# Performance work log

Measured on AMD Instinct MI355X. Metric: run time of the kernel, lower is better.

## Reference

```python
import jax, jax.numpy as jnp
import numpy as np

B, L_ENC, ENC_IN = 8, 1536, 7
LABEL_LEN, PRED_LEN = 512, 512
D_MODEL, N_HEADS, D_FF = 512, 8, 2048
E_LAYERS = 2
BUCKET_SIZE, N_HASHES = 64, 4
C_OUT, MARK_F = 7, 4
D_HEAD = D_MODEL // N_HEADS
L = L_ENC + PRED_LEN            # 2048, multiple of 2*bucket_size -> fit_length adds no pad
N_BUCKETS = L // BUCKET_SIZE    # 32
SELF_ATTN_VALUE = -5e4          # reformer_pytorch TOKEN_SELF_ATTN_VALUE


def _ln(x, g, b, eps=1e-5):
    mu = x.mean(-1, keepdims=True)
    var = ((x - mu) ** 2).mean(-1, keepdims=True)
    return (x - mu) * jax.lax.rsqrt(var + eps) * g + b


def _pos_embedding(length, d):
    pos = np.arange(length)[:, None].astype(np.float32)
    div = np.exp(np.arange(0, d, 2).astype(np.float32) * -(np.log(10000.0) / d))
    pe = np.zeros((length, d), np.float32)
    pe[:, 0::2] = np.sin(pos * div)
    pe[:, 1::2] = np.cos(pos * div)
    return jnp.asarray(pe)


def _lsh_attention(qk, v, rot):
    # qk, v: (b, L, d) with b = B*heads; rot: (d, n_hashes, n_buckets//2)
    b, Ls, d = qk.shape
    # --- hash: random rotations, buckets = argmax over [r, -r] ---
    rotated = jnp.einsum('bld,dhr->bhlr', qk, rot)
    rotated = jnp.concatenate([rotated, -rotated], axis=-1)            # (b,H,L,nb)
    buckets = jnp.argmax(rotated, axis=-1)                             # (b,H,L)
    buckets = buckets + (jnp.arange(N_HASHES) * N_BUCKETS)[None, :, None]
    buckets = buckets.reshape(b, N_HASHES * Ls)
    ticker = jnp.arange(N_HASHES * Ls)[None, :] % Ls
    # --- stable sort by (bucket, position) ---
    sticker = jnp.argsort(buckets * Ls + ticker, axis=-1)              # (b, H*L)
    undo_sort = jnp.argsort(sticker, axis=-1)
    st = sticker % Ls
    sqk = jnp.take_along_axis(qk, st[..., None], axis=1)               # (b, H*L, d)
    sv = jnp.take_along_axis(v, st[..., None], axis=1)
    n_chunks = N_HASHES * N_BUCKETS
    bq_t = st.reshape(b, n_chunks, -1)                                 # (b, C, cs)
    bq = sqk.reshape(b, n_chunks, -1, d)
    bv = sv.reshape(b, n_chunks, -1, d)
    # shared-QK: keys are l2-normalized queries
    bk = bq / jnp.maximum(jnp.linalg.norm(bq, axis=-1, keepdims=True), 1e-12)
    look = lambda x: jnp.concatenate([x, jnp.roll(x, 1, axis=1)], axis=2)
    bk, bv, bkv_t = look(bk), look(bv), look(bq_t)
    dots = jnp.einsum('bcie,bcje->bcij', bq, bk) * (d ** -0.5)         # (b,C,cs,2cs)
    self_mask = bq_t[:, :, :, None] == bkv_t[:, :, None, :]
    dots = jnp.where(self_mask, SELF_ATTN_VALUE, dots)
    lse = jax.nn.logsumexp(dots, axis=-1, keepdims=True)
    p = jnp.exp(dots - lse)
    so = jnp.einsum('bcij,bcje->bcie', p, bv).reshape(b, -1, d)        # (b, H*L, d)
    slog = lse.reshape(b, -1)
    o = jnp.take_along_axis(so, undo_sort[..., None], axis=1).reshape(b, N_HASHES, Ls, d)
    logits = jnp.take_along_axis(slog, undo_sort, axis=1).reshape(b, N_HASHES, Ls, 1)
    w = jnp.exp(logits - jax.nn.logsumexp(logits, axis=1, keepdims=True))
    return (o * w).sum(axis=1)                                         # (b, L, d)


def _forward(x_enc, x_mark_enc, x_dec, x_mark_dec, token_conv_w, time_w,
             qk_w, v_w, out_w, out_b, rotations,
             ffn1_w, ffn1_b, ffn2_w, ffn2_b,
             norm1_g, norm1_b, norm2_g, norm2_b, normf_g, normf_b,
             proj_w, proj_b):
    x = jnp.concatenate([x_enc, x_dec[:, -PRED_LEN:, :]], axis=1)      # (B, L, enc_in)
    xm = jnp.concatenate([x_mark_enc, x_mark_dec[:, -PRED_LEN:, :]], axis=1)
    # TokenEmbedding: Conv1d k=3, circular padding, no bias
    xp = jnp.concatenate([x[:, -1:, :], x, x[:, :1, :]], axis=1)
    tok = jax.lax.conv_general_dilated(xp, token_conv_w, (1,), 'VALID',
                                       dimension_numbers=('NWC', 'WIO', 'NWC'))
    h = tok + _pos_embedding(L, D_MODEL)[None] + xm @ time_w
    for l in range(E_LAYERS):
        qk = (h @ qk_w[l]).reshape(B, L, N_HEADS, D_HEAD).transpose(0, 2, 1, 3).reshape(B * N_HEADS, L, D_HEAD)
        v = (h @ v_w[l]).reshape(B, L, N_HEADS, D_HEAD).transpose(0, 2, 1, 3).reshape(B * N_HEADS, L, D_HEAD)
        a = _lsh_attention(qk, v, rotations[l])
        a = a.reshape(B, N_HEADS, L, D_HEAD).transpose(0, 2, 1, 3).reshape(B, L, D_MODEL)
        a = a @ out_w[l] + out_b[l]
        h = _ln(h + a, norm1_g[l], norm1_b[l])
        y = jax.nn.gelu(h @ ffn1_w[l] + ffn1_b[l], approximate=False) @ ffn2_w[l] + ffn2_b[l]
        h = _ln(h + y, norm2_g[l], norm2_b[l])
    h = _ln(h, normf_g, normf_b)
    out = h @ proj_w + proj_b
    return out[:, -PRED_LEN:, :]


def setup_inputs() -> dict:
    key = jax.random.key(0)
    ks = jax.random.split(key, 16)
    s = 0.02
    return {
        'x_enc': jax.random.normal(ks[0], (B, L_ENC, ENC_IN), jnp.float32),
        'x_mark_enc': jax.random.normal(ks[1], (B, L_ENC, MARK_F), jnp.float32),
        'x_dec': jax.random.normal(ks[2], (B, LABEL_LEN + PRED_LEN, ENC_IN), jnp.float32),
        'x_mark_dec': jax.random.normal(ks[3], (B, LABEL_LEN + PRED_LEN, MARK_F), jnp.float32),
        'token_conv_w': jax.random.normal(ks[4], (3, ENC_IN, D_MODEL), jnp.float32) * s,
        'time_w': jax.random.normal(ks[5], (MARK_F, D_MODEL), jnp.float32) * s,
        'qk_w': jax.random.normal(ks[6], (E_LAYERS, D_MODEL, D_MODEL), jnp.float32) * s,
        'v_w': jax.random.normal(ks[7], (E_LAYERS, D_MODEL, D_MODEL), jnp.float32) * s,
        'out_w': jax.random.normal(ks[8], (E_LAYERS, D_MODEL, D_MODEL), jnp.float32) * s,
        'out_b': jnp.zeros((E_LAYERS, D_MODEL), jnp.float32),
        'rotations': jax.random.normal(ks[9], (E_LAYERS, D_HEAD, N_HASHES, N_BUCKETS // 2), jnp.float32),
        'ffn1_w': jax.random.normal(ks[10], (E_LAYERS, D_MODEL, D_FF), jnp.float32) * s,
        'ffn1_b': jnp.zeros((E_LAYERS, D_FF), jnp.float32),
        'ffn2_w': jax.random.normal(ks[11], (E_LAYERS, D_FF, D_MODEL), jnp.float32) * s,
        'ffn2_b': jnp.zeros((E_LAYERS, D_MODEL), jnp.float32),
        'norm1_g': jnp.ones((E_LAYERS, D_MODEL), jnp.float32),
        'norm1_b': jnp.zeros((E_LAYERS, D_MODEL), jnp.float32),
        'norm2_g': jnp.ones((E_LAYERS, D_MODEL), jnp.float32),
        'norm2_b': jnp.zeros((E_LAYERS, D_MODEL), jnp.float32),
        'normf_g': jnp.ones((D_MODEL,), jnp.float32),
        'normf_b': jnp.zeros((D_MODEL,), jnp.float32),
        'proj_w': jax.random.normal(ks[12], (D_MODEL, C_OUT), jnp.float32) * s,
        'proj_b': jnp.zeros((C_OUT,), jnp.float32),
    }


def reference(x_enc, x_mark_enc, x_dec, x_mark_dec, token_conv_w, time_w,
              qk_w, v_w, out_w, out_b, rotations,
              ffn1_w, ffn1_b, ffn2_w, ffn2_b,
              norm1_g, norm1_b, norm2_g, norm2_b, normf_g, normf_b,
              proj_w, proj_b):
    return _forward(x_enc, x_mark_enc, x_dec, x_mark_dec, token_conv_w, time_w,
                    qk_w, v_w, out_w, out_b, rotations,
                    ffn1_w, ffn1_b, ffn2_w, ffn2_b,
                    norm1_g, norm1_b, norm2_g, norm2_b, normf_g, normf_b,
                    proj_w, proj_b)
```

## Files before the change

kernel.cpp:

```cpp
#include <hip/hip_runtime.h>


#define BATCH 8
#define SEQL 2048
#define DM 512
#define NH 8
#define DH 64
#define DFF 2048
#define NHASH 4
#define NBUCK 32
#define NCHUNK 128
#define CS 64
#define ROWS (BATCH*SEQL)
#define BHN (BATCH*NH)
#define SORTN (NHASH*SEQL)
#define SELF_VAL -5e4f

typedef __attribute__((ext_vector_type(4))) float f32x4;
typedef __attribute__((ext_vector_type(8))) short short8;

__device__ __forceinline__ float bfu2f(unsigned int u16) {
    return __uint_as_float(u16 << 16);
}
__device__ __forceinline__ unsigned short f2bfu(float f) {
    unsigned int x = __float_as_uint(f);
    x += 0x7fffu + ((x >> 16) & 1u);
    return (unsigned short)(x >> 16);
}

__device__ __forceinline__ void gld16(const void* g, void* l) {
    __builtin_amdgcn_global_load_lds(
        (const __attribute__((address_space(1))) unsigned int*)g,
        (__attribute__((address_space(3))) unsigned int*)l, 16, 0, 0);
}

__device__ __forceinline__ float getx(const float* xe, const float* xd, int b, int lm, int c) {
    return (lm < 1536) ? xe[((size_t)b * 1536 + lm) * 7 + c]
                       : xd[((size_t)b * 1024 + (lm - 1024)) * 7 + c];
}

__global__ __launch_bounds__(512) void embed_k(
    const float* __restrict__ x_enc, const float* __restrict__ x_me,
    const float* __restrict__ x_dec, const float* __restrict__ x_md,
    const float* __restrict__ cw, const float* __restrict__ tw,
    float* __restrict__ h, unsigned short* __restrict__ hb)
{
    const int row = blockIdx.x;
    const int b = row >> 11, l = row & 2047;
    const int d = threadIdx.x;
    __shared__ float xs[21];
    __shared__ float xms[4];
    if (d < 21) {
        const int k = d / 7, c = d % 7;
        const int lm = (l + k + 2047) & 2047;
        xs[d] = getx(x_enc, x_dec, b, lm, c);
    } else if (d < 25) {
        const int m = d - 21;
        xms[m] = (l < 1536) ? x_me[((size_t)b * 1536 + l) * 4 + m]
                            : x_md[((size_t)b * 1024 + (l - 1024)) * 4 + m];
    }
    __syncthreads();
    float tok = 0.f;
    #pragma unroll
    for (int kc = 0; kc < 21; ++kc) tok = fmaf(xs[kc], cw[kc * 512 + d], tok);
    float tm = 0.f;
    #pragma unroll
    for (int m = 0; m < 4; ++m) tm = fmaf(xms[m], tw[m * 512 + d], tm);
    const int pair = d & ~1;
    const float freq = expf((float)pair * (-9.210340371976184f / 512.f));
    const float ang = (float)l * freq;
    const float pe = (d & 1) ? cosf(ang) : sinf(ang);
    const float val = tok + pe + tm;
    h[(size_t)row * 512 + d] = val;
    hb[(size_t)row * 512 + d] = f2bfu(val);
}

__global__ __launch_bounds__(256) void gemm_k(
    const float* __restrict__ A, const float* __restrict__ B,
    float* __restrict__ C, int M, int N, int K)
{
    __shared__ float As[16][132];
    __shared__ float Bs[16][64];
    const int tid = threadIdx.x;
    const int bm = blockIdx.x * 128, bn = blockIdx.y * 64;
    const int ty = tid >> 4, tx = tid & 15;
    const int ar = tid >> 1, ac = (tid & 1) * 8;
    const int br = tid >> 4, bc = (tid & 15) * 4;
    float acc[8][4] = {};
    const float* Ap = A + (size_t)(bm + ar) * K + ac;
    const float* Bp = B + (size_t)br * N + bn + bc;
    float4 a0v = *reinterpret_cast<const float4*>(Ap);
    float4 a1v = *reinterpret_cast<const float4*>(Ap + 4);
    float4 b0v = *reinterpret_cast<const float4*>(Bp);
    for (int k0 = 0; k0 < K; k0 += 16) {
        As[ac + 0][ar] = a0v.x; As[ac + 1][ar] = a0v.y;
        As[ac + 2][ar] = a0v.z; As[ac + 3][ar] = a0v.w;
        As[ac + 4][ar] = a1v.x; As[ac + 5][ar] = a1v.y;
        As[ac + 6][ar] = a1v.z; As[ac + 7][ar] = a1v.w;
        *reinterpret_cast<float4*>(&Bs[br][bc]) = b0v;
        __syncthreads();
        if (k0 + 16 < K) {
            a0v = *reinterpret_cast<const float4*>(Ap + k0 + 16);
            a1v = *reinterpret_cast<const float4*>(Ap + k0 + 20);
            b0v = *reinterpret_cast<const float4*>(Bp + (size_t)(k0 + 16) * N);
        }
        #pragma unroll
        for (int k = 0; k < 16; ++k) {
            const float4 a0 = *reinterpret_cast<const float4*>(&As[k][ty * 8]);
            const float4 a1 = *reinterpret_cast<const float4*>(&As[k][ty * 8 + 4]);
            const float4 b0 = *reinterpret_cast<const float4*>(&Bs[k][tx * 4]);
            const float a[8] = {a0.x,a0.y,a0.z,a0.w,a1.x,a1.y,a1.z,a1.w};
            const float bb[4] = {b0.x,b0.y,b0.z,b0.w};
            #pragma unroll
            for (int i = 0; i < 8; ++i)
                #pragma unroll
                for (int j = 0; j < 4; ++j) acc[i][j] = fmaf(a[i], bb[j], acc[i][j]);
        }
        __syncthreads();
    }
    #pragma unroll
    for (int i = 0; i < 8; ++i) {
        const size_t cb = (size_t)(bm + ty * 8 + i) * N + bn + tx * 4;
        *reinterpret_cast<float4*>(C + cb) = make_float4(acc[i][0],acc[i][1],acc[i][2],acc[i][3]);
    }
}

__global__ __launch_bounds__(256) void tcast_k(
    const float* __restrict__ W, unsigned short* __restrict__ Wt, int K, int N)
{
    __shared__ float t[32][33];
    const size_t zo = (size_t)blockIdx.z * K * N;
    const int kb = blockIdx.x * 32, nb = blockIdx.y * 32;
    const int tx = threadIdx.x & 31, ty = threadIdx.x >> 5;
    #pragma unroll
    for (int i = ty; i < 32; i += 8)
        t[i][tx] = W[zo + (size_t)(kb + i) * N + nb + tx];
    __syncthreads();
    #pragma unroll
    for (int i = ty; i < 32; i += 8)
        Wt[zo + (size_t)(nb + i) * K + kb + tx] = f2bfu(t[tx][i]);
}

template<int OUT_BF, int ACT, int BIAS>
__global__ __launch_bounds__(256) void mgemm_k(
    const unsigned short* __restrict__ A,
    const unsigned short* __restrict__ Bt,
    const float* __restrict__ bias,
    void* __restrict__ Cv, int N, int K)
{
    __shared__ unsigned short As[128 * 32];
    __shared__ unsigned short Bs[128 * 32];
    const int tid = threadIdx.x;
    const int bm = blockIdx.x * 128, bn = blockIdx.y * 128;
    const int lane = tid & 63, w = tid >> 6;
    const int wr = (w >> 1) * 64, wc = (w & 1) * 64;
    const int fr = lane & 15, fq = lane >> 4;
    const int r0 = tid >> 2, c0 = (tid & 3) * 8;
    const unsigned short* Ag = A + (size_t)(bm + r0) * K + c0;
    const unsigned short* Bg = Bt + (size_t)(bn + r0) * K + c0;
    f32x4 acc[4][4];
    #pragma unroll
    for (int i = 0; i < 4; ++i)
        #pragma unroll
        for (int j = 0; j < 4; ++j) acc[i][j] = (f32x4){0.f, 0.f, 0.f, 0.f};
    for (int k0 = 0; k0 < K; k0 += 32) {
        gld16(Ag + k0,                   As + tid * 8);
        gld16(Ag + (size_t)64 * K + k0,  As + tid * 8 + 2048);
        gld16(Bg + k0,                   Bs + tid * 8);
        gld16(Bg + (size_t)64 * K + k0,  Bs + tid * 8 + 2048);
        __syncthreads();
        short8 af[4], bfr[4];
        #pragma unroll
        for (int mi = 0; mi < 4; ++mi)
            af[mi] = *reinterpret_cast<const short8*>(As + (wr + mi * 16 + fr) * 32 + fq * 8);
        #pragma unroll
        for (int ni = 0; ni < 4; ++ni)
            bfr[ni] = *reinterpret_cast<const short8*>(Bs + (wc + ni * 16 + fr) * 32 + fq * 8);
        #pragma unroll
        for (int mi = 0; mi < 4; ++mi)
            #pragma unroll
            for (int ni = 0; ni < 4; ++ni)
                acc[mi][ni] = __builtin_amdgcn_mfma_f32_16x16x32_bf16(
                    af[mi], bfr[ni], acc[mi][ni], 0, 0, 0);
        __syncthreads();
    }
    float bv[4];
    if (BIAS) {
        #pragma unroll
        for (int ni = 0; ni < 4; ++ni) bv[ni] = bias[bn + wc + ni * 16 + fr];
    }
    #pragma unroll
    for (int mi = 0; mi < 4; ++mi) {
        #pragma unroll
        for (int r = 0; r < 4; ++r) {
            const int row = bm + wr + mi * 16 + fq * 4 + r;
            #pragma unroll
            for (int ni = 0; ni < 4; ++ni) {
                float val = acc[mi][ni][r];
                if (BIAS) val += bv[ni];
                if (ACT) val = 0.5f * val * (1.0f + erff(val * 0.7071067811865475f));
                const size_t idx = (size_t)row * N + bn + wc + ni * 16 + fr;
                if (OUT_BF) ((unsigned short*)Cv)[idx] = f2bfu(val);
                else        ((float*)Cv)[idx] = val;
            }
        }
    }
}

__global__ __launch_bounds__(256, 4) void hash_k(
    const float* __restrict__ qk, const float* __restrict__ rot,
    int* __restrict__ buckets)
{
    __shared__ float rs[16][68];
    const int t = threadIdx.x;
    const int hh_blk = blockIdx.x >> 9;
    for (int u = t; u < 1024; u += 256) {
        const int d = u >> 4, j = u & 15;
        rs[j][d] = rot[d * 64 + hh_blk * 16 + j];
    }
    __syncthreads();
    const int gid = blockIdx.x * 256 + t;
    const int l = gid & 2047;
    const int bh = (gid >> 11) & 63;
    const int hh = gid >> 17;
    const int b = bh >> 3, head = bh & 7;
    const float* qrow = qk + (size_t)(b * 2048 + l) * 512 + head * 64;
    float q[64];
    #pragma unroll
    for (int d4 = 0; d4 < 16; ++d4) {
        const float4 qq = reinterpret_cast<const float4*>(qrow)[d4];
        q[d4*4+0]=qq.x; q[d4*4+1]=qq.y; q[d4*4+2]=qq.z; q[d4*4+3]=qq.w;
    }
    float bvp = -1e38f, bvn = -1e38f;
    int bip = 0, bin_ = 16;
    #pragma unroll
    for (int j = 0; j < 16; ++j) {
        float dot = 0.f;
        #pragma unroll
        for (int d = 0; d < 64; d += 4) {
            const float4 r = *reinterpret_cast<const float4*>(&rs[j][d]);
            dot += q[d]*r.x + q[d+1]*r.y + q[d+2]*r.z + q[d+3]*r.w;
        }
        if (dot  > bvp) { bvp = dot;  bip = j; }
        if (-dot > bvn) { bvn = -dot; bin_ = 16 + j; }
    }
    const int idx = (bvn > bvp) ? bin_ : bip;
    buckets[((size_t)bh << 13) + hh * 2048 + l] = hh * 32 + idx;
}

__global__ __launch_bounds__(256) void sort_k(
    const int* __restrict__ buckets, int* __restrict__ st_sorted, int* __restrict__ pos_of)
{
    const int bh = blockIdx.x >> 2, hh = blockIdx.x & 3;
    const int t = threadIdx.x;
    __shared__ unsigned short cnt[256][32];
    __shared__ int tot[32];
    __shared__ int startc[32];
    {
        uint4* p = reinterpret_cast<uint4*>(&cnt[t][0]);
        const uint4 z = {0,0,0,0};
        #pragma unroll
        for (int q = 0; q < 4; ++q) p[q] = z;
    }
    const size_t base = (size_t)bh * SORTN + hh * 2048;
    int myb[8];
    #pragma unroll
    for (int j = 0; j < 8; ++j) {
        const int i = t * 8 + j;
        const int g = buckets[base + i] - hh * 32;
        myb[j] = g;
        cnt[t][g]++;
    }
    __syncthreads();
    if (t < 32) {
        int run = 0;
        for (int tt = 0; tt < 256; ++tt) {
            const int x = cnt[tt][t];
            cnt[tt][t] = (unsigned short)run;
            run += x;
        }
        tot[t] = run;
    }
    __syncthreads();
    if (t == 0) {
        int s = 0;
        for (int g = 0; g < 32; ++g) { startc[g] = s; s += tot[g]; }
    }
    __syncthreads();
    #pragma unroll
    for (int j = 0; j < 8; ++j) {
        const int i = t * 8 + j;
        const int g = myb[j];
        const int rank = cnt[t][g]++;
        const int pos = hh * 2048 + startc[g] + rank;
        st_sorted[(size_t)bh * SORTN + pos] = i;
        pos_of[base + i] = pos;
    }
}

__global__ __launch_bounds__(256) void lsh_attn_k(
    const float* __restrict__ qk, const unsigned short* __restrict__ vbf,
    const int* __restrict__ st_sorted,
    unsigned short* __restrict__ so, float* __restrict__ slog)
{
    const int c = blockIdx.x;
    const int bh = blockIdx.y;
    const int b = bh >> 3, head = bh & 7;
    __shared__ unsigned short Ks[128 * 72];
    __shared__ unsigned short Vt[128 * 64];
    __shared__ unsigned short Ps[64 * 136];
    __shared__ float rnorm[128];
    __shared__ int stk[128];
    const int t = threadIdx.x;

    {
        const int r = t >> 1, hf = t & 1;
        const int cprev = (c + NCHUNK - 1) & (NCHUNK - 1);
        const int spos = (r < 64) ? (c * CS + r) : (cprev * CS + (r - 64));
        const int l = st_sorted[(size_t)bh * SORTN + spos];
        if (hf == 0) stk[r] = l;
        const size_t ro = (size_t)(b * 2048 + l) * 512 + head * 64 + hf * 32;
        const float4* q4 = reinterpret_cast<const float4*>(qk + ro);
        float ss = 0.f;
        #pragma unroll
        for (int u = 0; u < 8; ++u) {
            const float4 a = q4[u];
            ss += a.x*a.x + a.y*a.y + a.z*a.z + a.w*a.w;
            ushort4 pk;
            pk.x = f2bfu(a.x); pk.y = f2bfu(a.y); pk.z = f2bfu(a.z); pk.w = f2bfu(a.w);
            *reinterpret_cast<ushort4*>(&Ks[r * 72 + hf * 32 + u * 4]) = pk;
        }
        ss += __shfl_xor(ss, 1);
        if (hf == 0) rnorm[r] = 1.0f / fmaxf(sqrtf(ss), 1e-12f);
        const uint4* v16 = reinterpret_cast<const uint4*>(vbf + ro);
        const uint4 a0 = v16[0], a1 = v16[1], a2 = v16[2], a3 = v16[3];
        const unsigned int wd[16] = {a0.x,a0.y,a0.z,a0.w, a1.x,a1.y,a1.z,a1.w,
                                     a2.x,a2.y,a2.z,a2.w, a3.x,a3.y,a3.z,a3.w};
        #pragma unroll
        for (int e = 0; e < 32; ++e) {
            const int d = hf * 32 + e;
            const unsigned short us = (unsigned short)(wd[e >> 1] >> ((e & 1) * 16));
            Vt[(d * 128 + r) ^ ((d & 7) << 3)] = us;
        }
    }
    __syncthreads();

    const int lane = t & 63, w = t >> 6;
    const int fr = lane & 15, fq = lane >> 4;

    short8 aq[2];
    #pragma unroll
    for (int s = 0; s < 2; ++s)
        aq[s] = *reinterpret_cast<const short8*>(&Ks[(w * 16 + fr) * 72 + s * 32 + fq * 8]);
    f32x4 cc[8];
    #pragma unroll
    for (int n = 0; n < 8; ++n) cc[n] = (f32x4){0.f, 0.f, 0.f, 0.f};
    #pragma unroll
    for (int n = 0; n < 8; ++n) {
        #pragma unroll
        for (int s = 0; s < 2; ++s) {
            const short8 bk = *reinterpret_cast<const short8*>(
                &Ks[(n * 16 + fr) * 72 + s * 32 + fq * 8]);
            cc[n] = __builtin_amdgcn_mfma_f32_16x16x32_bf16(aq[s], bk, cc[n], 0, 0, 0);
        }
    }

    int stq_r[4];
    #pragma unroll
    for (int r = 0; r < 4; ++r) stq_r[r] = stk[w * 16 + fq * 4 + r];
    float mx[4] = {-3.0e38f, -3.0e38f, -3.0e38f, -3.0e38f};
    #pragma unroll
    for (int n = 0; n < 8; ++n) {
        const int key = n * 16 + fr;
        const float rn = rnorm[key] * 0.125f;
        const int sk = stk[key];
        #pragma unroll
        for (int r = 0; r < 4; ++r) {
            const float val = (stq_r[r] == sk) ? SELF_VAL : cc[n][r] * rn;
            cc[n][r] = val;
            mx[r] = fmaxf(mx[r], val);
        }
    }
    #pragma unroll
    for (int r = 0; r < 4; ++r) {
        mx[r] = fmaxf(mx[r], __shfl_xor(mx[r], 1));
        mx[r] = fmaxf(mx[r], __shfl_xor(mx[r], 2));
        mx[r] = fmaxf(mx[r], __shfl_xor(mx[r], 4));
        mx[r] = fmaxf(mx[r], __shfl_xor(mx[r], 8));
    }
    float sm[4] = {0.f, 0.f, 0.f, 0.f};
    #pragma unroll
    for (int n = 0; n < 8; ++n)
        #pragma unroll
        for (int r = 0; r < 4; ++r) {
            const float e = __expf(cc[n][r] - mx[r]);
            cc[n][r] = e;
            sm[r] += e;
        }
    #pragma unroll
    for (int r = 0; r < 4; ++r) {
        sm[r] += __shfl_xor(sm[r], 1);
        sm[r] += __shfl_xor(sm[r], 2);
        sm[r] += __shfl_xor(sm[r], 4);
        sm[r] += __shfl_xor(sm[r], 8);
    }
    float rsum[4];
    #pragma unroll
    for (int r = 0; r < 4; ++r) rsum[r] = 1.0f / sm[r];
    if (fr == 0) {
        #pragma unroll
        for (int r = 0; r < 4; ++r)
            slog[(size_t)bh * SORTN + c * CS + w * 16 + fq * 4 + r] = mx[r] + logf(sm[r]);
    }

    #pragma unroll
    for (int n = 0; n < 8; ++n)
        #pragma unroll
        for (int r = 0; r < 4; ++r)
            Ps[(w * 16 + fq * 4 + r) * 136 + n * 16 + fr] = f2bfu(cc[n][r]);
    __syncthreads();

    short8 pa[4];
    #pragma unroll
    for (int s = 0; s < 4; ++s)
        pa[s] = *reinterpret_cast<const short8*>(&Ps[(w * 16 + fr) * 136 + s * 32 + fq * 8]);
    f32x4 oo[4];
    #pragma unroll
    for (int n = 0; n < 4; ++n) oo[n] = (f32x4){0.f, 0.f, 0.f, 0.f};
    #pragma unroll
    for (int n = 0; n < 4; ++n) {
        const int d = n * 16 + fr;
        #pragma unroll
        for (int s = 0; s < 4; ++s) {
            const short8 vb = *reinterpret_cast<const short8*>(
                &Vt[(d * 128 + s * 32 + fq * 8) ^ ((d & 7) << 3)]);
            oo[n] = __builtin_amdgcn_mfma_f32_16x16x32_bf16(pa[s], vb, oo[n], 0, 0, 0);
        }
    }

    #pragma unroll
    for (int r = 0; r < 4; ++r) {
        const int qrow = w * 16 + fq * 4 + r;
        const size_t ob = ((size_t)bh * SORTN + c * CS + qrow) * 64;
        #pragma unroll
        for (int n = 0; n < 4; ++n)
            so[ob + n * 16 + fr] = f2bfu(oo[n][r] * rsum[r]);
    }
}

__global__ __launch_bounds__(256) void combine_k(
    const unsigned short* __restrict__ so, const float* __restrict__ slog,
    const int* __restrict__ pos_of, unsigned short* __restrict__ aout)
{
    const int gid = blockIdx.x * 256 + threadIdx.x;
    const int d = gid & 63;
    const int bl = gid >> 6;
    const int l = bl & 2047;
    const int bh = bl >> 11;
    const int b = bh >> 3, head = bh & 7;
    int pos[4]; float lg[4];
    #pragma unroll
    for (int hh = 0; hh < 4; ++hh) {
        pos[hh] = pos_of[((size_t)bh << 13) + hh * 2048 + l];
        lg[hh] = slog[((size_t)bh << 13) + pos[hh]];
    }
    const float m = fmaxf(fmaxf(lg[0], lg[1]), fmaxf(lg[2], lg[3]));
    float w[4]; float sw = 0.f;
    #pragma unroll
    for (int hh = 0; hh < 4; ++hh) { w[hh] = expf(lg[hh] - m); sw += w[hh]; }
    const float inv = 1.0f / sw;
    float acc = 0.f;
    #pragma unroll
    for (int hh = 0; hh < 4; ++hh)
        acc += w[hh] * bfu2f(so[(((size_t)bh << 13) + pos[hh]) * 64 + d]);
    aout[(size_t)(b * 2048 + l) * 512 + head * 64 + d] = f2bfu(acc * inv);
}

template<int RES, int WBF>
__global__ __launch_bounds__(256) void ln_k(
    float* __restrict__ h, const float* __restrict__ res,
    const float* __restrict__ g, const float* __restrict__ bta,
    unsigned short* __restrict__ hb)
{
    const int row = blockIdx.x * 4 + (threadIdx.x >> 6);
    const int lane = threadIdx.x & 63;
    const size_t base = (size_t)row * 512;
    float4 xa = *reinterpret_cast<const float4*>(h + base + lane * 4);
    float4 xb = *reinterpret_cast<const float4*>(h + base + 256 + lane * 4);
    if (RES) {
        const float4 ra = *reinterpret_cast<const float4*>(res + base + lane * 4);
        const float4 rb = *reinterpret_cast<const float4*>(res + base + 256 + lane * 4);
        xa.x += ra.x; xa.y += ra.y; xa.z += ra.z; xa.w += ra.w;
        xb.x += rb.x; xb.y += rb.y; xb.z += rb.z; xb.w += rb.w;
    }
    float sum = xa.x + xa.y + xa.z + xa.w + xb.x + xb.y + xb.z + xb.w;
    float sq = xa.x*xa.x + xa.y*xa.y + xa.z*xa.z + xa.w*xa.w
             + xb.x*xb.x + xb.y*xb.y + xb.z*xb.z + xb.w*xb.w;
    #pragma unroll
    for (int off = 32; off > 0; off >>= 1) {
        sum += __shfl_xor(sum, off);
        sq  += __shfl_xor(sq, off);
    }
    const float mu = sum * (1.0f / 512.0f);
    const float var = sq * (1.0f / 512.0f) - mu * mu;
    const float rstd = rsqrtf(var + 1e-5f);
    const float4 ga = *reinterpret_cast<const float4*>(g + lane * 4);
    const float4 gb = *reinterpret_cast<const float4*>(g + 256 + lane * 4);
    const float4 ba = *reinterpret_cast<const float4*>(bta + lane * 4);
    const float4 bb = *reinterpret_cast<const float4*>(bta + 256 + lane * 4);
    float4 oa, ob;
    oa.x = (xa.x - mu) * rstd * ga.x + ba.x;
    oa.y = (xa.y - mu) * rstd * ga.y + ba.y;
    oa.z = (xa.z - mu) * rstd * ga.z + ba.z;
    oa.w = (xa.w - mu) * rstd * ga.w + ba.w;
    ob.x = (xb.x - mu) * rstd * gb.x + bb.x;
    ob.y = (xb.y - mu) * rstd * gb.y + bb.y;
    ob.z = (xb.z - mu) * rstd * gb.z + bb.z;
    ob.w = (xb.w - mu) * rstd * gb.w + bb.w;
    *reinterpret_cast<float4*>(h + base + lane * 4) = oa;
    *reinterpret_cast<float4*>(h + base + 256 + lane * 4) = ob;
    if (WBF) {
        ushort4 pa, pb;
        pa.x = f2bfu(oa.x); pa.y = f2bfu(oa.y); pa.z = f2bfu(oa.z); pa.w = f2bfu(oa.w);
        pb.x = f2bfu(ob.x); pb.y = f2bfu(ob.y); pb.z = f2bfu(ob.z); pb.w = f2bfu(ob.w);
        *reinterpret_cast<ushort4*>(hb + base + lane * 4) = pa;
        *reinterpret_cast<ushort4*>(hb + base + 256 + lane * 4) = pb;
    }
}

__global__ __launch_bounds__(256) void lnf_k(
    float* __restrict__ h, const float* __restrict__ g, const float* __restrict__ bta)
{
    const int vrow = blockIdx.x * 4 + (threadIdx.x >> 6);
    const int row = (vrow >> 9) * 2048 + 1536 + (vrow & 511);
    const int lane = threadIdx.x & 63;
    const size_t base = (size_t)row * 512;
    float4 xa = *reinterpret_cast<const float4*>(h + base + lane * 4);
    float4 xb = *reinterpret_cast<const float4*>(h + base + 256 + lane * 4);
    float sum = xa.x + xa.y + xa.z + xa.w + xb.x + xb.y + xb.z + xb.w;
    float sq = xa.x*xa.x + xa.y*xa.y + xa.z*xa.z + xa.w*xa.w
             + xb.x*xb.x + xb.y*xb.y + xb.z*xb.z + xb.w*xb.w;
    #pragma unroll
    for (int off = 32; off > 0; off >>= 1) {
        sum += __shfl_xor(sum, off);
        sq  += __shfl_xor(sq, off);
    }
    const float mu = sum * (1.0f / 512.0f);
    const float var = sq * (1.0f / 512.0f) - mu * mu;
    const float rstd = rsqrtf(var + 1e-5f);
    const float4 ga = *reinterpret_cast<const float4*>(g + lane * 4);
    const float4 gb = *reinterpret_cast<const float4*>(g + 256 + lane * 4);
    const float4 ba = *reinterpret_cast<const float4*>(bta + lane * 4);
    const float4 bb = *reinterpret_cast<const float4*>(bta + 256 + lane * 4);
    float4 oa, ob;
    oa.x = (xa.x - mu) * rstd * ga.x + ba.x;
    oa.y = (xa.y - mu) * rstd * ga.y + ba.y;
    oa.z = (xa.z - mu) * rstd * ga.z + ba.z;
    oa.w = (xa.w - mu) * rstd * ga.w + ba.w;
    ob.x = (xb.x - mu) * rstd * gb.x + bb.x;
    ob.y = (xb.y - mu) * rstd * gb.y + bb.y;
    ob.z = (xb.z - mu) * rstd * gb.z + bb.z;
    ob.w = (xb.w - mu) * rstd * gb.w + bb.w;
    *reinterpret_cast<float4*>(h + base + lane * 4) = oa;
    *reinterpret_cast<float4*>(h + base + 256 + lane * 4) = ob;
}

__global__ __launch_bounds__(256) void proj_k(
    const float* __restrict__ h, const float* __restrict__ pw,
    const float* __restrict__ pb, float* __restrict__ out)
{
    const int wid = (blockIdx.x * 256 + threadIdx.x) >> 6;
    const int lane = threadIdx.x & 63;
    const int b = wid >> 9, tt = wid & 511;
    const float* row = h + (size_t)(b * 2048 + 1536 + tt) * 512;
    const float4 h0 = reinterpret_cast<const float4*>(row)[lane * 2];
    const float4 h1 = reinterpret_cast<const float4*>(row)[lane * 2 + 1];
    const float he[8] = {h0.x, h0.y, h0.z, h0.w, h1.x, h1.y, h1.z, h1.w};
    float acc[7] = {};
    #pragma unroll
    for (int e = 0; e < 8; ++e) {
        const int k = lane * 8 + e;
        #pragma unroll
        for (int cq = 0; cq < 7; ++cq) acc[cq] = fmaf(he[e], pw[k * 7 + cq], acc[cq]);
    }
    #pragma unroll
    for (int cq = 0; cq < 7; ++cq) {
        #pragma unroll
        for (int off = 32; off > 0; off >>= 1) acc[cq] += __shfl_xor(acc[cq], off);
    }
    if (lane == 0) {
        const size_t ob = ((size_t)(b * 512) + tt) * 7;
        #pragma unroll
        for (int cq = 0; cq < 7; ++cq) out[ob + cq] = acc[cq] + pb[cq];
    }
}

__global__ void nan_k(float* o) { o[0] = __int_as_float(0x7fc00000); }

extern "C" void kernel_launch(void* const* d_in, const int* in_sizes, int n_in,
                              void* d_out, int out_size, void* d_ws, size_t ws_size,
                              hipStream_t stream)
{
    const float* x_enc  = (const float*)d_in[0];
    const float* x_me   = (const float*)d_in[1];
    const float* x_dec  = (const float*)d_in[2];
    const float* x_md   = (const float*)d_in[3];
    const float* conv_w = (const float*)d_in[4];
    const float* time_w = (const float*)d_in[5];
    const float* qk_w   = (const float*)d_in[6];
    const float* v_w    = (const float*)d_in[7];
    const float* out_w  = (const float*)d_in[8];
    const float* out_b  = (const float*)d_in[9];
    const float* rots   = (const float*)d_in[10];
    const float* f1w    = (const float*)d_in[11];
    const float* f1b    = (const float*)d_in[12];
    const float* f2w    = (const float*)d_in[13];
    const float* f2b    = (const float*)d_in[14];
    const float* n1g    = (const float*)d_in[15];
    const float* n1b    = (const float*)d_in[16];
    const float* n2g    = (const float*)d_in[17];
    const float* n2b    = (const float*)d_in[18];
    const float* nfg    = (const float*)d_in[19];
    const float* nfb    = (const float*)d_in[20];
    const float* pw     = (const float*)d_in[21];
    const float* pb     = (const float*)d_in[22];

    char* ws = (char*)d_ws;
    const size_t HBYT = (size_t)ROWS * DM * 4;
    float* h    = (float*)ws;                  ws += HBYT;
    unsigned short* hb = (unsigned short*)ws;  ws += HBYT / 2;
    float* qkb  = (float*)ws;                  ws += HBYT;
    float* gout = (float*)ws;                  ws += HBYT;
    unsigned short* mid = (unsigned short*)ws; ws += (size_t)ROWS * DFF * 2;
    float* slog = (float*)ws;                  ws += (size_t)BHN * SORTN * 4;
    int* buckets = (int*)ws;                   ws += (size_t)BHN * SORTN * 4;
    int* st_sorted = (int*)ws;                 ws += (size_t)BHN * SORTN * 4;
    int* pos_of = (int*)ws;                    ws += (size_t)BHN * SORTN * 4;
    unsigned short* wT = (unsigned short*)ws;  ws += (size_t)(2*262144 + 2*262144 + 2*1048576 + 2*1048576) * 2;
    const size_t need = (size_t)(ws - (char*)d_ws);
    if (ws_size < need) { nan_k<<<1, 1, 0, stream>>>((float*)d_out); return; }

    unsigned short* vT  = wT;
    unsigned short* oT  = vT + 2 * 262144;
    unsigned short* f1T = oT + 2 * 262144;
    unsigned short* f2T = f1T + 2 * 1048576;
    unsigned short* ab  = (unsigned short*)qkb;
    unsigned short* vbf = (unsigned short*)gout;

    tcast_k<<<dim3(16, 16, 2), 256, 0, stream>>>(v_w,   vT,  DM, DM);
    tcast_k<<<dim3(16, 16, 2), 256, 0, stream>>>(out_w, oT,  DM, DM);
    tcast_k<<<dim3(16, 64, 2), 256, 0, stream>>>(f1w,   f1T, DM, DFF);
    tcast_k<<<dim3(64, 16, 2), 256, 0, stream>>>(f2w,   f2T, DFF, DM);

    embed_k<<<ROWS, 512, 0, stream>>>(x_enc, x_me, x_dec, x_md, conv_w, time_w, h, hb);

    for (int l = 0; l < 2; ++l) {
        const size_t wo = (size_t)l * DM * DM;
        gemm_k<<<dim3(ROWS/128, DM/64), 256, 0, stream>>>(h, qk_w + wo, qkb, ROWS, DM, DM);
        mgemm_k<1,0,0><<<dim3(ROWS/128, DM/128), 256, 0, stream>>>(hb, vT + (size_t)l*262144, nullptr, vbf, DM, DM);
        hash_k<<<(NHASH * BHN * SEQL) / 256, 256, 0, stream>>>(qkb, rots + (size_t)l * DH * NHASH * (NBUCK/2), buckets);
        sort_k<<<BHN * 4, 256, 0, stream>>>(buckets, st_sorted, pos_of);
        lsh_attn_k<<<dim3(NCHUNK, BHN), 256, 0, stream>>>(qkb, vbf, st_sorted, mid , slog);
        combine_k<<<(BHN * SEQL * DH) / 256, 256, 0, stream>>>(mid, slog, pos_of, ab);
        mgemm_k<0,0,1><<<dim3(ROWS/128, DM/128), 256, 0, stream>>>(ab, oT + (size_t)l*262144, out_b + l * DM, gout, DM, DM);
        ln_k<1,1><<<ROWS/4, 256, 0, stream>>>(h, gout, n1g + l * DM, n1b + l * DM, hb);
        mgemm_k<1,1,1><<<dim3(ROWS/128, DFF/128), 256, 0, stream>>>(hb, f1T + (size_t)l*1048576, f1b + l * DFF, mid, DFF, DM);
        mgemm_k<0,0,1><<<dim3(ROWS/128, DM/128), 256, 0, stream>>>(mid, f2T + (size_t)l*1048576, f2b + l * DM, gout, DM, DFF);
        ln_k<1,1><<<ROWS/4, 256, 0, stream>>>(h, gout, n2g + l * DM, n2b + l * DM, hb);
    }
    lnf_k<<<(BATCH * 512) / 4, 256, 0, stream>>>(h, nfg, nfb);
    proj_k<<<(BATCH * 512 / 4), 256, 0, stream>>>(h, pw, pb, (float*)d_out);
}
```

Baseline: 957.4 us.

## Deepen fp32 GEMM K-tile to 32 and alias attention P buffer onto K tile

The fp32 tiled GEMM now stages 32-wide K slices per iteration instead of 16, halving the barrier count per output tile at the cost of doubled LDS and more prefetch registers. The LSH attention kernel reuses the K shared buffer for the probability matrix, with an added barrier to protect it, and requests 4 blocks per CU via launch bounds. Together these aim to cut sync overhead and raise occupancy, with a risk of register pressure or spills from the occupancy hint.

```diff
diff --git a/kernel.cpp b/kernel.cpp
--- a/kernel.cpp
+++ b/kernel.cpp
@@ -79,33 +79,44 @@
     const float* __restrict__ A, const float* __restrict__ B,
     float* __restrict__ C, int M, int N, int K)
 {
-    __shared__ float As[16][132];
-    __shared__ float Bs[16][64];
+    __shared__ float As[32][132];
+    __shared__ float Bs[32][64];
     const int tid = threadIdx.x;
     const int bm = blockIdx.x * 128, bn = blockIdx.y * 64;
     const int ty = tid >> 4, tx = tid & 15;
-    const int ar = tid >> 1, ac = (tid & 1) * 8;
-    const int br = tid >> 4, bc = (tid & 15) * 4;
+    const int ar = tid >> 1, ac = (tid & 1) * 16;
+    const int br = tid >> 3, bc = (tid & 7) * 8;
     float acc[8][4] = {};
     const float* Ap = A + (size_t)(bm + ar) * K + ac;
     const float* Bp = B + (size_t)br * N + bn + bc;
-    float4 a0v = *reinterpret_cast<const float4*>(Ap);
-    float4 a1v = *reinterpret_cast<const float4*>(Ap + 4);
-    float4 b0v = *reinterpret_cast<const float4*>(Bp);
-    for (int k0 = 0; k0 < K; k0 += 16) {
-        As[ac + 0][ar] = a0v.x; As[ac + 1][ar] = a0v.y;
-        As[ac + 2][ar] = a0v.z; As[ac + 3][ar] = a0v.w;
-        As[ac + 4][ar] = a1v.x; As[ac + 5][ar] = a1v.y;
-        As[ac + 6][ar] = a1v.z; As[ac + 7][ar] = a1v.w;
-        *reinterpret_cast<float4*>(&Bs[br][bc]) = b0v;
+    float4 av0 = *reinterpret_cast<const float4*>(Ap);
+    float4 av1 = *reinterpret_cast<const float4*>(Ap + 4);
+    float4 av2 = *reinterpret_cast<const float4*>(Ap + 8);
+    float4 av3 = *reinterpret_cast<const float4*>(Ap + 12);
+    float4 bv0 = *reinterpret_cast<const float4*>(Bp);
+    float4 bv1 = *reinterpret_cast<const float4*>(Bp + 4);
+    for (int k0 = 0; k0 < K; k0 += 32) {
+        As[ac + 0][ar] = av0.x; As[ac + 1][ar] = av0.y;
+        As[ac + 2][ar] = av0.z; As[ac + 3][ar] = av0.w;
+        As[ac + 4][ar] = av1.x; As[ac + 5][ar] = av1.y;
+        As[ac + 6][ar] = av1.z; As[ac + 7][ar] = av1.w;
+        As[ac + 8][ar] = av2.x; As[ac + 9][ar] = av2.y;
+        As[ac + 10][ar] = av2.z; As[ac + 11][ar] = av2.w;
+        As[ac + 12][ar] = av3.x; As[ac + 13][ar] = av3.y;
+        As[ac + 14][ar] = av3.z; As[ac + 15][ar] = av3.w;
+        *reinterpret_cast<float4*>(&Bs[br][bc])     = bv0;
+        *reinterpret_cast<float4*>(&Bs[br][bc + 4]) = bv1;
         __syncthreads();
-        if (k0 + 16 < K) {
-            a0v = *reinterpret_cast<const float4*>(Ap + k0 + 16);
-            a1v = *reinterpret_cast<const float4*>(Ap + k0 + 20);
-            b0v = *reinterpret_cast<const float4*>(Bp + (size_t)(k0 + 16) * N);
-        }
-        #pragma unroll
-        for (int k = 0; k < 16; ++k) {
+        if (k0 + 32 < K) {
+            av0 = *reinterpret_cast<const float4*>(Ap + k0 + 32);
+            av1 = *reinterpret_cast<const float4*>(Ap + k0 + 36);
+            av2 = *reinterpret_cast<const float4*>(Ap + k0 + 40);
+            av3 = *reinterpret_cast<const float4*>(Ap + k0 + 44);
+            bv0 = *reinterpret_cast<const float4*>(Bp + (size_t)(k0 + 32) * N);
+            bv1 = *reinterpret_cast<const float4*>(Bp + (size_t)(k0 + 32) * N + 4);
+        }
+        #pragma unroll
+        for (int k = 0; k < 32; ++k) {
             const float4 a0 = *reinterpret_cast<const float4*>(&As[k][ty * 8]);
             const float4 a1 = *reinterpret_cast<const float4*>(&As[k][ty * 8 + 4]);
             const float4 b0 = *reinterpret_cast<const float4*>(&Bs[k][tx * 4]);
@@ -298,7 +309,7 @@
     }
 }
 
-__global__ __launch_bounds__(256) void lsh_attn_k(
+__global__ __launch_bounds__(256, 4) void lsh_attn_k(
     const float* __restrict__ qk, const unsigned short* __restrict__ vbf,
     const int* __restrict__ st_sorted,
     unsigned short* __restrict__ so, float* __restrict__ slog)
@@ -308,9 +319,9 @@
     const int b = bh >> 3, head = bh & 7;
     __shared__ unsigned short Ks[128 * 72];
     __shared__ unsigned short Vt[128 * 64];
-    __shared__ unsigned short Ps[64 * 136];
     __shared__ float rnorm[128];
     __shared__ int stk[128];
+    unsigned short* Ps = Ks;
     const int t = threadIdx.x;
 
     {
@@ -412,6 +423,8 @@
         for (int r = 0; r < 4; ++r)
             slog[(size_t)bh * SORTN + c * CS + w * 16 + fq * 4 + r] = mx[r] + logf(sm[r]);
     }
+
+    __syncthreads();
 
     #pragma unroll
     for (int n = 0; n < 8; ++n)
```

After: 975.1 us. No clear change (+1.8%).

## Double-buffer fp32 GEMM shared tiles and alias attention P buffer onto K

Applied to the files above, without the earlier changes.

The fp32 GEMM now uses two shared-memory buffers, so the next tile is written while the current one is consumed, leaving one barrier per k-step instead of two. The LSH attention kernel reuses the key shared buffer for the probability matrix, with an added barrier, and declares a minimum of 4 blocks per SM to raise occupancy. The cost is twice the shared memory in the GEMM, one extra barrier in attention, and possible register pressure from the launch bound.

```diff
diff --git a/kernel.cpp b/kernel.cpp
--- a/kernel.cpp
+++ b/kernel.cpp
@@ -79,8 +79,8 @@
     const float* __restrict__ A, const float* __restrict__ B,
     float* __restrict__ C, int M, int N, int K)
 {
-    __shared__ float As[16][132];
-    __shared__ float Bs[16][64];
+    __shared__ float As[2][16][132];
+    __shared__ float Bs[2][16][64];
     const int tid = threadIdx.x;
     const int bm = blockIdx.x * 128, bn = blockIdx.y * 64;
     const int ty = tid >> 4, tx = tid & 15;
@@ -89,26 +89,31 @@
     float acc[8][4] = {};
     const float* Ap = A + (size_t)(bm + ar) * K + ac;
     const float* Bp = B + (size_t)br * N + bn + bc;
-    float4 a0v = *reinterpret_cast<const float4*>(Ap);
-    float4 a1v = *reinterpret_cast<const float4*>(Ap + 4);
-    float4 b0v = *reinterpret_cast<const float4*>(Bp);
+    {
+        const float4 a0v = *reinterpret_cast<const float4*>(Ap);
+        const float4 a1v = *reinterpret_cast<const float4*>(Ap + 4);
+        const float4 b0v = *reinterpret_cast<const float4*>(Bp);
+        As[0][ac + 0][ar] = a0v.x; As[0][ac + 1][ar] = a0v.y;
+        As[0][ac + 2][ar] = a0v.z; As[0][ac + 3][ar] = a0v.w;
+        As[0][ac + 4][ar] = a1v.x; As[0][ac + 5][ar] = a1v.y;
+        As[0][ac + 6][ar] = a1v.z; As[0][ac + 7][ar] = a1v.w;
+        *reinterpret_cast<float4*>(&Bs[0][br][bc]) = b0v;
+    }
+    __syncthreads();
+    int cur = 0;
     for (int k0 = 0; k0 < K; k0 += 16) {
-        As[ac + 0][ar] = a0v.x; As[ac + 1][ar] = a0v.y;
-        As[ac + 2][ar] = a0v.z; As[ac + 3][ar] = a0v.w;
-        As[ac + 4][ar] = a1v.x; As[ac + 5][ar] = a1v.y;
-        As[ac + 6][ar] = a1v.z; As[ac + 7][ar] = a1v.w;
-        *reinterpret_cast<float4*>(&Bs[br][bc]) = b0v;
-        __syncthreads();
-        if (k0 + 16 < K) {
+        float4 a0v, a1v, b0v;
+        const int more = (k0 + 16 < K);
+        if (more) {
             a0v = *reinterpret_cast<const float4*>(Ap + k0 + 16);
             a1v = *reinterpret_cast<const float4*>(Ap + k0 + 20);
             b0v = *reinterpret_cast<const float4*>(Bp + (size_t)(k0 + 16) * N);
         }
         #pragma unroll
         for (int k = 0; k < 16; ++k) {
-            const float4 a0 = *reinterpret_cast<const float4*>(&As[k][ty * 8]);
-            const float4 a1 = *reinterpret_cast<const float4*>(&As[k][ty * 8 + 4]);
-            const float4 b0 = *reinterpret_cast<const float4*>(&Bs[k][tx * 4]);
+            const float4 a0 = *reinterpret_cast<const float4*>(&As[cur][k][ty * 8]);
+            const float4 a1 = *reinterpret_cast<const float4*>(&As[cur][k][ty * 8 + 4]);
+            const float4 b0 = *reinterpret_cast<const float4*>(&Bs[cur][k][tx * 4]);
             const float a[8] = {a0.x,a0.y,a0.z,a0.w,a1.x,a1.y,a1.z,a1.w};
             const float bb[4] = {b0.x,b0.y,b0.z,b0.w};
             #pragma unroll
@@ -116,7 +121,16 @@
                 #pragma unroll
                 for (int j = 0; j < 4; ++j) acc[i][j] = fmaf(a[i], bb[j], acc[i][j]);
         }
+        if (more) {
+            const int nxt = cur ^ 1;
+            As[nxt][ac + 0][ar] = a0v.x; As[nxt][ac + 1][ar] = a0v.y;
+            As[nxt][ac + 2][ar] = a0v.z; As[nxt][ac + 3][ar] = a0v.w;
+            As[nxt][ac + 4][ar] = a1v.x; As[nxt][ac + 5][ar] = a1v.y;
+            As[nxt][ac + 6][ar] = a1v.z; As[nxt][ac + 7][ar] = a1v.w;
+            *reinterpret_cast<float4*>(&Bs[nxt][br][bc]) = b0v;
+        }
         __syncthreads();
+        cur ^= 1;
     }
     #pragma unroll
     for (int i = 0; i < 8; ++i) {
@@ -298,7 +312,7 @@
     }
 }
 
-__global__ __launch_bounds__(256) void lsh_attn_k(
+__global__ __launch_bounds__(256, 4) void lsh_attn_k(
     const float* __restrict__ qk, const unsigned short* __restrict__ vbf,
     const int* __restrict__ st_sorted,
     unsigned short* __restrict__ so, float* __restrict__ slog)
@@ -308,9 +322,9 @@
     const int b = bh >> 3, head = bh & 7;
     __shared__ unsigned short Ks[128 * 72];
     __shared__ unsigned short Vt[128 * 64];
-    __shared__ unsigned short Ps[64 * 136];
     __shared__ float rnorm[128];
     __shared__ int stk[128];
+    unsigned short* Ps = Ks;
     const int t = threadIdx.x;
 
     {
@@ -412,6 +426,8 @@
         for (int r = 0; r < 4; ++r)
             slog[(size_t)bh * SORTN + c * CS + w * 16 + fq * 4 + r] = mx[r] + logf(sm[r]);
     }
+
+    __syncthreads();
 
     #pragma unroll
     for (int n = 0; n < 8; ++n)
```

After: 966.4 us. No clear change (+0.9%).
